# Optimization experiments

Hardware: AMD Instinct MI355X
Metric: run time of the kernel (lower is better)

## Reference

```python
import jax, jax.numpy as jnp
import numpy as np
from jax import lax

DN = ('NCHW', 'OIHW', 'NCHW')

def _dwsep(x, dw, pw_w, pw_b, stride):
    # depthwise: groups = in_channels, kernel (C,1,3,3)
    y = lax.conv_general_dilated(x, dw, (stride, stride), [(1, 1), (1, 1)],
                                 dimension_numbers=DN, feature_group_count=x.shape[1])
    # pointwise 1x1
    y = lax.conv_general_dilated(y, pw_w, (1, 1), 'VALID', dimension_numbers=DN)
    return y + pw_b[None, :, None, None]

def setup_inputs() -> dict:
    key = jax.random.key(0)
    ks = jax.random.split(key, 16)
    s = 0.1
    inp = {
        'flow_raw': jax.random.normal(ks[0], (32, 2, 480, 640), jnp.float32),
        'dw1': jax.random.normal(ks[1], (5, 1, 3, 3), jnp.float32) * s,
        'pw1_w': jax.random.normal(ks[2], (32, 5, 1, 1), jnp.float32) * s,
        'pw1_b': jnp.zeros((32,), jnp.float32),
        'dw2': jax.random.normal(ks[3], (32, 1, 3, 3), jnp.float32) * s,
        'pw2_w': jax.random.normal(ks[4], (64, 32, 1, 1), jnp.float32) * s,
        'pw2_b': jnp.zeros((64,), jnp.float32),
        'dw3': jax.random.normal(ks[5], (64, 1, 3, 3), jnp.float32) * s,
        'pw3_w': jax.random.normal(ks[6], (64, 64, 1, 1), jnp.float32) * s,
        'pw3_b': jnp.zeros((64,), jnp.float32),
        'attn_w': jax.random.normal(ks[7], (1, 64, 1, 1), jnp.float32) * s,
        'attn_b': jnp.zeros((1,), jnp.float32),
        'mlp1_w': jax.random.normal(ks[8], (32, 64), jnp.float32) * s,
        'mlp1_b': jnp.zeros((32,), jnp.float32),
        'mlp2_w': jax.random.normal(ks[9], (3, 32), jnp.float32) * s,
        'mlp2_b': jnp.zeros((3,), jnp.float32),
        'w_ih': jax.random.normal(ks[10], (96, 3), jnp.float32) * s,
        'w_hh': jax.random.normal(ks[11], (96, 32), jnp.float32) * s,
        'b_ih': jnp.zeros((96,), jnp.float32),
        'b_hh': jnp.zeros((96,), jnp.float32),
        'fc_w': jnp.zeros((3, 32), jnp.float32),  # gru_fc init to zero in torch code
        'fc_b': jnp.zeros((3,), jnp.float32),
    }
    return inp

def reference(flow_raw, dw1, pw1_w, pw1_b, dw2, pw2_w, pw2_b, dw3, pw3_w, pw3_b,
              attn_w, attn_b, mlp1_w, mlp1_b, mlp2_w, mlp2_b,
              w_ih, w_hh, b_ih, b_hh, fc_w, fc_b):
    B, _, H, W = flow_raw.shape
    # coordinate channels (x, y, r^2)
    y = jnp.linspace(-1.0, 1.0, H)
    x = jnp.linspace(-1.0, 1.0, W)
    yy, xx = jnp.meshgrid(y, x, indexing='ij')
    coords = jnp.stack([xx, yy, xx**2 + yy**2], axis=0)            # (3,H,W)
    coords_b = jnp.broadcast_to(coords[None], (B, 3, H, W))
    inp = jnp.concatenate([flow_raw, coords_b], axis=1)            # (B,5,H,W)

    f = jax.nn.elu(_dwsep(inp, dw1, pw1_w, pw1_b, 2))              # (B,32,H/2,W/2)
    f = jax.nn.elu(_dwsep(f, dw2, pw2_w, pw2_b, 2))                # (B,64,H/4,W/4)
    f = jax.nn.elu(_dwsep(f, dw3, pw3_w, pw3_b, 2))                # (B,64,H/8,W/8)

    # attention pooling
    logits = jnp.einsum('bchw,oc->bohw', f, attn_w[:, :, 0, 0]) + attn_b[None, :, None, None]
    Bs, _, Hs, Ws = logits.shape
    w = jax.nn.softmax(logits.reshape(Bs, Hs * Ws), axis=-1)       # (B, HW)
    pooled = jnp.einsum('bcn,bn->bc', f.reshape(Bs, 64, Hs * Ws), w)  # (B,64)

    # omega MLP
    h1 = jax.nn.elu(pooled @ mlp1_w.T + mlp1_b)
    omega_inst = h1 @ mlp2_w.T + mlp2_b                            # (B,3)

    # single-step GRU, h0 = 0 (PyTorch gate order: r, z, n)
    h0 = jnp.zeros((B, 32), flow_raw.dtype)
    gi = omega_inst @ w_ih.T + b_ih                                # (B,96)
    gh = h0 @ w_hh.T + b_hh
    i_r, i_z, i_n = jnp.split(gi, 3, axis=-1)
    h_r, h_z, h_n = jnp.split(gh, 3, axis=-1)
    r = jax.nn.sigmoid(i_r + h_r)
    z = jax.nn.sigmoid(i_z + h_z)
    n = jnp.tanh(i_n + r * h_n)
    h = (1.0 - z) * n + z * h0                                     # (B,32)

    delta_omega = h @ fc_w.T + fc_b
    return omega_inst + delta_omega
```

## Files before the change

kernel.cpp:

```cpp
#include <hip/hip_runtime.h>
#include <hip/hip_bf16.h>

#define H0 480
#define W0 640
#define H1 240
#define W1 320
#define H2 120
#define W2 160
#define H3 60
#define W3 80

#define W_PW1T  0
#define W_PW2T  160
#define W_PW3T  2208
#define WBUF_BYTES 65536

#define F2_PB (64 * H2 * W2)
#define F3_PB (64 * H3 * W3)

#define TH 8
#define TW 32
#define TILES_W 5
#define TILES_H 15
#define TILES_PB 75
#define F1COLS 65
#define NP 1105
#define LROW 66
#define LCH 1122

typedef float v2f __attribute__((ext_vector_type(2)));

__global__ __launch_bounds__(256) void k_cvt(
    const float* __restrict__ pw1, const float* __restrict__ pw2,
    const float* __restrict__ pw3, float* __restrict__ wb)
{
    int t = threadIdx.x;
    for (int i = t; i < 160;  i += 256) { int o = i / 5,  c = i % 5;  wb[W_PW1T + c*32 + o] = pw1[i]; }
    for (int i = t; i < 2048; i += 256) { int o = i >> 5, c = i & 31; wb[W_PW2T + c*64 + o] = pw2[i]; }
    for (int i = t; i < 4096; i += 256) { int o = i >> 6, c = i & 63; wb[W_PW3T + c*64 + o] = pw3[i]; }
}

__global__ __launch_bounds__(256, 4) void k_fuse12(
    const float* __restrict__ flow, const float* __restrict__ dw1,
    const float* __restrict__ b1, const float* __restrict__ dw2,
    const float* __restrict__ b2, const float* __restrict__ wb,
    float* __restrict__ out)
{
    __shared__ float f1buf[8 * LCH];

    const int t = threadIdx.x;
    const int bid = blockIdx.x;
    const int b = bid / TILES_PB;
    const int tile = bid - b * TILES_PB;
    const int oh0 = (tile / TILES_W) * TH;
    const int ow0 = (tile % TILES_W) * TW;

    const float sx = 2.f / (W0 - 1), sy = 2.f / (H0 - 1);

    float cs2[3], rs3[3], cs4[3], rs4[3];
    #pragma unroll
    for (int k = 0; k < 3; k++) {
        cs2[k] = dw1[18+k]   + dw1[21+k]   + dw1[24+k];
        rs3[k] = dw1[27+3*k] + dw1[28+3*k] + dw1[29+3*k];
        cs4[k] = dw1[36+k]   + dw1[39+k]   + dw1[42+k];
        rs4[k] = dw1[36+3*k] + dw1[37+3*k] + dw1[38+3*k];
    }
    const float ax2 = 2.f * sx, ay2 = 2.f * sy;
    float ex[3], fyc[3];
    #pragma unroll
    for (int k = 0; k < 3; k++) { ex[k] = sx*(float)(k-1) - 1.f; fyc[k] = sy*(float)(k-1) - 1.f; }
    const float AX1 = ax2*(cs2[0]+cs2[1]+cs2[2]);
    const float AX0 = cs2[0]*ex[0]+cs2[1]*ex[1]+cs2[2]*ex[2];
    const float AY1 = ay2*(rs3[0]+rs3[1]+rs3[2]);
    const float AY0 = rs3[0]*fyc[0]+rs3[1]*fyc[1]+rs3[2]*fyc[2];
    const float GX2 = ax2*ax2*(cs4[0]+cs4[1]+cs4[2]);
    const float GX1 = 2.f*ax2*(cs4[0]*ex[0]+cs4[1]*ex[1]+cs4[2]*ex[2]);
    const float GX0 = cs4[0]*ex[0]*ex[0]+cs4[1]*ex[1]*ex[1]+cs4[2]*ex[2]*ex[2];
    const float GY2 = ay2*ay2*(rs4[0]+rs4[1]+rs4[2]);
    const float GY1 = 2.f*ay2*(rs4[0]*fyc[0]+rs4[1]*fyc[1]+rs4[2]*fyc[2]);
    const float GY0 = rs4[0]*fyc[0]*fyc[0]+rs4[1]*fyc[1]*fyc[1]+rs4[2]*fyc[2]*fyc[2];

    float dd[5][5];
    float vmf[5];
    int   widx[5];
    const float* fb0 = flow + (size_t)(b*2) * (H0*W0);
    const float* fb1 = fb0 + (size_t)(H0*W0);

    #pragma unroll
    for (int i = 0; i < 5; i++) {
        int p = t + i*256; if (p > NP-1) p = NP-1;
        int tr = p / F1COLS;
        int tc = p - tr * F1COLS;
        widx[i] = tr*LROW + (tc & 1)*33 + (tc >> 1);
        int fr = 2*oh0 - 1 + tr;
        int fc = 2*ow0 - 1 + tc;
        vmf[i] = (fr >= 0 && fc >= 0) ? 1.f : 0.f;
        if (fr >= 1 && fc >= 1) {
            const float* r0 = fb0 + (size_t)(2*fr - 1) * W0 + (2*fc - 1);
            const float* r1 = fb1 + (size_t)(2*fr - 1) * W0 + (2*fc - 1);
            float a0 = 0.f, a1 = 0.f;
            #pragma unroll
            for (int ky = 0; ky < 3; ky++)
                #pragma unroll
                for (int kx = 0; kx < 3; kx++) {
                    a0 = fmaf(dw1[ky*3+kx],   r0[ky*W0+kx], a0);
                    a1 = fmaf(dw1[9+ky*3+kx], r1[ky*W0+kx], a1);
                }
            dd[i][0] = a0; dd[i][1] = a1;
            float fcf = (float)fc, frf = (float)fr;
            dd[i][2] = fmaf(AX1, fcf, AX0);
            dd[i][3] = fmaf(AY1, frf, AY0);
            dd[i][4] = fmaf(fmaf(GX2, fcf, GX1), fcf, GX0)
                     + fmaf(fmaf(GY2, frf, GY1), frf, GY0);
        } else {
            int frc = fr < 0 ? 0 : fr, fcc = fc < 0 ? 0 : fc;
            int ih0 = 2*frc - 1, iw0 = 2*fcc - 1;
            float mh[3] = { ih0 >= 0 ? 1.f : 0.f, 1.f, 1.f };
            float mw[3] = { iw0 >= 0 ? 1.f : 0.f, 1.f, 1.f };
            int ihx[3] = { ih0 < 0 ? 0 : ih0, ih0 + 1, ih0 + 2 };
            int iwx[3] = { iw0 < 0 ? 0 : iw0, iw0 + 1, iw0 + 2 };
            float a0 = 0.f, a1 = 0.f;
            #pragma unroll
            for (int ky = 0; ky < 3; ky++) {
                const float* rp0 = fb0 + (size_t)ihx[ky] * W0;
                const float* rp1 = fb1 + (size_t)ihx[ky] * W0;
                #pragma unroll
                for (int kx = 0; kx < 3; kx++) {
                    float m = mh[ky]*mw[kx];
                    a0 = fmaf(dw1[ky*3+kx],   m * rp0[iwx[kx]], a0);
                    a1 = fmaf(dw1[9+ky*3+kx], m * rp1[iwx[kx]], a1);
                }
            }
            dd[i][0] = a0; dd[i][1] = a1;
            float axv = 0.f, ayv = 0.f, arv = 0.f;
            #pragma unroll
            for (int ky = 0; ky < 3; ky++) {
                float yv = fmaf((float)(ih0 + ky), sy, -1.f);
                #pragma unroll
                for (int kx = 0; kx < 3; kx++) {
                    float xv = fmaf((float)(iw0 + kx), sx, -1.f);
                    float m = mh[ky]*mw[kx];
                    axv = fmaf(dw1[18 + ky*3 + kx], m * xv, axv);
                    ayv = fmaf(dw1[27 + ky*3 + kx], m * yv, ayv);
                    arv = fmaf(dw1[36 + ky*3 + kx], m * (xv*xv + yv*yv), arv);
                }
            }
            dd[i][2] = axv; dd[i][3] = ayv; dd[i][4] = arv;
        }
    }

    v2f acc2[32];
    #pragma unroll
    for (int o = 0; o < 32; o++) acc2[o] = *(const v2f*)(b2 + 2*o);

    const int lr = t >> 5, lc = t & 31;
    const int rbase = 2*lr*LROW + lc;

    for (int cc = 0; cc < 4; cc++) {
        #pragma unroll
        for (int j = 0; j < 8; j++) {
            int c = cc*8 + j;
            float w10 = wb[W_PW1T + c];
            float w11 = wb[W_PW1T + 32 + c];
            float w12 = wb[W_PW1T + 64 + c];
            float w13 = wb[W_PW1T + 96 + c];
            float w14 = wb[W_PW1T + 128 + c];
            float bc = b1[c];
            #pragma unroll
            for (int i = 0; i < 5; i++) {
                float v = bc;
                v = fmaf(w10, dd[i][0], v);
                v = fmaf(w11, dd[i][1], v);
                v = fmaf(w12, dd[i][2], v);
                v = fmaf(w13, dd[i][3], v);
                v = fmaf(w14, dd[i][4], v);
                float f = v > 0.f ? v : (__expf(v) - 1.f);
                f *= vmf[i];
                if (i < 4)               f1buf[j*LCH + widx[i]] = f;
                else if (t < NP - 1024)  f1buf[j*LCH + widx[4]] = f;
            }
        }
        __syncthreads();
        #pragma unroll
        for (int j = 0; j < 8; j++) {
            int c = cc*8 + j;
            const float* w9 = dw2 + c*9;
            const float* fp = f1buf + j*LCH + rbase;
            float dv = 0.f;
            #pragma unroll
            for (int r = 0; r < 3; r++) {
                dv = fmaf(w9[r*3+0], fp[r*LROW],      dv);
                dv = fmaf(w9[r*3+1], fp[r*LROW + 33], dv);
                dv = fmaf(w9[r*3+2], fp[r*LROW + 1],  dv);
            }
            const v2f* wr2 = (const v2f*)(wb + W_PW2T + c*64);
            v2f dvv = { dv, dv };
            #pragma unroll
            for (int o = 0; o < 32; o++)
                acc2[o] = __builtin_elementwise_fma(wr2[o], dvv, acc2[o]);
        }
        __syncthreads();
    }

    const int oh = oh0 + lr, ow = ow0 + lc;
    size_t obase = ((size_t)b * 64) * (H2*W2) + (size_t)oh * W2 + ow;
    #pragma unroll
    for (int o = 0; o < 32; o++) {
        float va = acc2[o].x, vb2 = acc2[o].y;
        out[obase + (size_t)(2*o)   * (H2*W2)] = va  > 0.f ? va  : (__expf(va)  - 1.f);
        out[obase + (size_t)(2*o+1) * (H2*W2)] = vb2 > 0.f ? vb2 : (__expf(vb2) - 1.f);
    }
}

__global__ __launch_bounds__(256, 4) void k_stage3(
    const float* __restrict__ in, const float* __restrict__ dw3,
    const float* __restrict__ b3, const float* __restrict__ wb,
    float* __restrict__ out)
{
    int idx = blockIdx.x * 256 + threadIdx.x;
    int ow = idx % W3; int tmp = idx / W3; int oh = tmp % H3; int b = tmp / H3;
    int ih0 = 2*oh - 1, iw0 = 2*ow - 1;
    float mh[3] = { ih0 >= 0 ? 1.f : 0.f, 1.f, 1.f };
    float mw[3] = { iw0 >= 0 ? 1.f : 0.f, 1.f, 1.f };
    int ihx[3] = { ih0 < 0 ? 0 : ih0, ih0 + 1, ih0 + 2 };
    int iwx[3] = { iw0 < 0 ? 0 : iw0, iw0 + 1, iw0 + 2 };
    float m9[9];
    int off[9];
    #pragma unroll
    for (int ky = 0; ky < 3; ky++)
        #pragma unroll
        for (int kx = 0; kx < 3; kx++) {
            m9[ky*3 + kx] = mh[ky] * mw[kx];
            off[ky*3 + kx] = ihx[ky]*W2 + iwx[kx];
        }

    v2f acc2[32];
    #pragma unroll
    for (int o = 0; o < 32; o++) acc2[o] = *(const v2f*)(b3 + 2*o);

    const float* inb = in + (size_t)b * F2_PB;
    for (int c = 0; c < 64; c++) {
        const float* g = inb + (size_t)c * (H2*W2);
        const float* w9 = dw3 + c*9;
        float dv = 0.f;
        #pragma unroll
        for (int p = 0; p < 9; p++)
            dv = fmaf(w9[p], m9[p] * g[off[p]], dv);
        const v2f* wr2 = (const v2f*)(wb + W_PW3T + c*64);
        v2f dvv = { dv, dv };
        #pragma unroll
        for (int o = 0; o < 32; o++)
            acc2[o] = __builtin_elementwise_fma(wr2[o], dvv, acc2[o]);
    }

    size_t obase = ((size_t)b * 64) * (H3*W3) + (size_t)oh*W3 + ow;
    #pragma unroll
    for (int o = 0; o < 32; o++) {
        float va = acc2[o].x, vb2 = acc2[o].y;
        out[obase + (size_t)(2*o)  *(H3*W3)] = va  > 0.f ? va  : (__expf(va)  - 1.f);
        out[obase + (size_t)(2*o+1)*(H3*W3)] = vb2 > 0.f ? vb2 : (__expf(vb2) - 1.f);
    }
}

__global__ __launch_bounds__(1024) void k_head(
    const float* __restrict__ f3,
    const float* __restrict__ attn_w, const float* __restrict__ attn_b,
    const float* __restrict__ mlp1_w, const float* __restrict__ mlp1_b,
    const float* __restrict__ mlp2_w, const float* __restrict__ mlp2_b,
    const float* __restrict__ w_ih, const float* __restrict__ b_ih,
    const float* __restrict__ b_hh,
    const float* __restrict__ fc_w, const float* __restrict__ fc_b,
    float* __restrict__ out)
{
    const int N  = H3 * W3;
    const int N4 = N / 4;
    __shared__ float s_w[H3 * W3];
    __shared__ float s_attn[64];
    __shared__ float s_redm[16];
    __shared__ float s_reds[16];
    __shared__ float s_inv[1];
    __shared__ float s_pooled[64];
    __shared__ float s_h1[32];
    __shared__ float s_om[3];
    __shared__ float s_h[32];

    int t = threadIdx.x, b = blockIdx.x;
    int lane = t & 63, wid = t >> 6;
    if (t < 64) s_attn[t] = attn_w[t];
    __syncthreads();

    const float4* fb4 = (const float4*)(f3 + (size_t)b * F3_PB);
    float ab = attn_b[0];

    float lmax = -1e30f;
    for (int n4 = t; n4 < N4; n4 += 1024) {
        float4 l = make_float4(ab, ab, ab, ab);
        #pragma unroll 8
        for (int c = 0; c < 64; c++) {
            float4 v = fb4[c * N4 + n4];
            float a = s_attn[c];
            l.x = fmaf(a, v.x, l.x); l.y = fmaf(a, v.y, l.y);
            l.z = fmaf(a, v.z, l.z); l.w = fmaf(a, v.w, l.w);
        }
        ((float4*)s_w)[n4] = l;
        lmax = fmaxf(lmax, fmaxf(fmaxf(l.x, l.y), fmaxf(l.z, l.w)));
    }
    #pragma unroll
    for (int off = 32; off; off >>= 1) lmax = fmaxf(lmax, __shfl_down(lmax, off, 64));
    if (lane == 0) s_redm[wid] = lmax;
    __syncthreads();
    {
        float m = s_redm[0];
        #pragma unroll
        for (int i = 1; i < 16; i++) m = fmaxf(m, s_redm[i]);
        lmax = m;
    }

    float lsum = 0.f;
    for (int n = t; n < N; n += 1024) { float e = __expf(s_w[n] - lmax); s_w[n] = e; lsum += e; }
    #pragma unroll
    for (int off = 32; off; off >>= 1) lsum += __shfl_down(lsum, off, 64);
    if (lane == 0) s_reds[wid] = lsum;
    __syncthreads();
    if (t == 0) {
        float s = 0.f;
        #pragma unroll
        for (int i = 0; i < 16; i++) s += s_reds[i];
        s_inv[0] = 1.f / s;
    }
    __syncthreads();
    float invS = s_inv[0];

    const float4* sw4 = (const float4*)s_w;
    for (int c = wid; c < 64; c += 16) {
        float s = 0.f;
        for (int i = lane; i < N4; i += 64) {
            float4 v = fb4[c * N4 + i];
            float4 w = sw4[i];
            s = fmaf(v.x, w.x, s); s = fmaf(v.y, w.y, s);
            s = fmaf(v.z, w.z, s); s = fmaf(v.w, w.w, s);
        }
        #pragma unroll
        for (int off = 32; off; off >>= 1) s += __shfl_down(s, off, 64);
        if (lane == 0) s_pooled[c] = s * invS;
    }
    __syncthreads();

    if (t < 32) {
        float a = mlp1_b[t];
        #pragma unroll 8
        for (int c = 0; c < 64; c++) a = fmaf(mlp1_w[t*64 + c], s_pooled[c], a);
        s_h1[t] = a > 0.f ? a : (__expf(a) - 1.f);
    }
    __syncthreads();
    if (t < 3) {
        float a = mlp2_b[t];
        for (int j = 0; j < 32; j++) a = fmaf(mlp2_w[t*32 + j], s_h1[j], a);
        s_om[t] = a;
    }
    __syncthreads();
    if (t < 32) {
        float gr = b_ih[t], gz = b_ih[32 + t], gn = b_ih[64 + t];
        #pragma unroll
        for (int k = 0; k < 3; k++) {
            float ok = s_om[k];
            gr = fmaf(w_ih[t*3 + k],        ok, gr);
            gz = fmaf(w_ih[(32 + t)*3 + k], ok, gz);
            gn = fmaf(w_ih[(64 + t)*3 + k], ok, gn);
        }
        float hr = b_hh[t], hz = b_hh[32 + t], hn = b_hh[64 + t];
        float r = 1.f / (1.f + __expf(-(gr + hr)));
        float z = 1.f / (1.f + __expf(-(gz + hz)));
        float nn = tanhf(gn + r * hn);
        s_h[t] = (1.f - z) * nn;
    }
    __syncthreads();
    if (t < 3) {
        float dl = fc_b[t];
        for (int j = 0; j < 32; j++) dl = fmaf(fc_w[t*32 + j], s_h[j], dl);
        out[b*3 + t] = s_om[t] + dl;
    }
}

extern "C" void kernel_launch(void* const* d_in, const int* in_sizes, int n_in,
                              void* d_out, int out_size, void* d_ws, size_t ws_size,
                              hipStream_t stream)
{
    const float* flow = (const float*)d_in[0];
    float* wb = (float*)d_ws;

    float* f2 = (float*)((char*)d_ws + WBUF_BYTES);
    float* f3 = f2 + (size_t)32 * F2_PB;

    k_cvt<<<1, 256, 0, stream>>>(
        (const float*)d_in[2], (const float*)d_in[5], (const float*)d_in[8], wb);

    k_fuse12<<<32 * TILES_PB, 256, 0, stream>>>(
        flow, (const float*)d_in[1], (const float*)d_in[3],
        (const float*)d_in[4], (const float*)d_in[6], wb, f2);

    k_stage3<<<(32*H3*W3)/256, 256, 0, stream>>>(
        f2, (const float*)d_in[7], (const float*)d_in[9], wb, f3);

    k_head<<<32, 1024, 0, stream>>>(f3,
        (const float*)d_in[10], (const float*)d_in[11],
        (const float*)d_in[12], (const float*)d_in[13],
        (const float*)d_in[14], (const float*)d_in[15],
        (const float*)d_in[16], (const float*)d_in[18],
        (const float*)d_in[19], (const float*)d_in[20],
        (const float*)d_in[21], (float*)d_out);
}
```

Baseline: 331.7 us.

## Fuse attention logits into stage3 and split head into parallel softmax/pool kernels

Computes the attention logit per pixel inside the stage-3 epilogue, so the head no longer re-reads all 64 channels of f3 to form logits. The old single 32-block head kernel is split into a softmax kernel, a pooling kernel with one block per (batch, channel), and a small MLP/GRU tail kernel, which spreads the pooling reduction across far more blocks. It also lowers the k_fuse12 occupancy hint from 4 to 3 waves. The split adds two kernel launches and a global-memory round trip for the logits.

```diff
diff --git a/kernel.cpp b/kernel.cpp
--- a/kernel.cpp
+++ b/kernel.cpp
@@ -17,6 +17,7 @@
 
 #define F2_PB (64 * H2 * W2)
 #define F3_PB (64 * H3 * W3)
+#define N3    (H3 * W3)
 
 #define TH 8
 #define TW 32
@@ -40,7 +41,7 @@
     for (int i = t; i < 4096; i += 256) { int o = i >> 6, c = i & 63; wb[W_PW3T + c*64 + o] = pw3[i]; }
 }
 
-__global__ __launch_bounds__(256, 4) void k_fuse12(
+__global__ __launch_bounds__(256, 3) void k_fuse12(
     const float* __restrict__ flow, const float* __restrict__ dw1,
     const float* __restrict__ b1, const float* __restrict__ dw2,
     const float* __restrict__ b2, const float* __restrict__ wb,
@@ -215,7 +216,8 @@
 __global__ __launch_bounds__(256, 4) void k_stage3(
     const float* __restrict__ in, const float* __restrict__ dw3,
     const float* __restrict__ b3, const float* __restrict__ wb,
-    float* __restrict__ out)
+    const float* __restrict__ attn_w, const float* __restrict__ attn_b,
+    float* __restrict__ out, float* __restrict__ lg)
 {
     int idx = blockIdx.x * 256 + threadIdx.x;
     int ow = idx % W3; int tmp = idx / W3; int oh = tmp % H3; int b = tmp / H3;
@@ -254,17 +256,76 @@
     }
 
     size_t obase = ((size_t)b * 64) * (H3*W3) + (size_t)oh*W3 + ow;
+    float logit = attn_b[0];
     #pragma unroll
     for (int o = 0; o < 32; o++) {
         float va = acc2[o].x, vb2 = acc2[o].y;
-        out[obase + (size_t)(2*o)  *(H3*W3)] = va  > 0.f ? va  : (__expf(va)  - 1.f);
-        out[obase + (size_t)(2*o+1)*(H3*W3)] = vb2 > 0.f ? vb2 : (__expf(vb2) - 1.f);
-    }
-}
-
-__global__ __launch_bounds__(1024) void k_head(
-    const float* __restrict__ f3,
-    const float* __restrict__ attn_w, const float* __restrict__ attn_b,
+        float ea = va  > 0.f ? va  : (__expf(va)  - 1.f);
+        float eb = vb2 > 0.f ? vb2 : (__expf(vb2) - 1.f);
+        out[obase + (size_t)(2*o)  *(H3*W3)] = ea;
+        out[obase + (size_t)(2*o+1)*(H3*W3)] = eb;
+        logit = fmaf(attn_w[2*o],   ea, logit);
+        logit = fmaf(attn_w[2*o+1], eb, logit);
+    }
+    lg[b*N3 + oh*W3 + ow] = logit;
+}
+
+__global__ __launch_bounds__(256) void k_softmax(
+    float* __restrict__ lg, float* __restrict__ invs)
+{
+    int b = blockIdx.x, t = threadIdx.x;
+    int lane = t & 63, wid = t >> 6;
+    __shared__ float sm[4], ss[4];
+    float* base = lg + b*N3;
+
+    float m = -1e30f;
+    for (int n = t; n < N3; n += 256) m = fmaxf(m, base[n]);
+    #pragma unroll
+    for (int o = 32; o; o >>= 1) m = fmaxf(m, __shfl_down(m, o, 64));
+    if (lane == 0) sm[wid] = m;
+    __syncthreads();
+    m = fmaxf(fmaxf(sm[0], sm[1]), fmaxf(sm[2], sm[3]));
+
+    float s = 0.f;
+    for (int n = t; n < N3; n += 256) {
+        float e = __expf(base[n] - m);
+        base[n] = e;
+        s += e;
+    }
+    #pragma unroll
+    for (int o = 32; o; o >>= 1) s += __shfl_down(s, o, 64);
+    if (lane == 0) ss[wid] = s;
+    __syncthreads();
+    if (t == 0) invs[b] = 1.f / (ss[0] + ss[1] + ss[2] + ss[3]);
+}
+
+__global__ __launch_bounds__(256) void k_pool(
+    const float* __restrict__ f3, const float* __restrict__ lg,
+    const float* __restrict__ invs, float* __restrict__ pooled)
+{
+    int bc = blockIdx.x;
+    int b = bc >> 6, c = bc & 63;
+    int t = threadIdx.x, lane = t & 63, wid = t >> 6;
+    __shared__ float sr[4];
+
+    const float4* f = (const float4*)(f3 + (size_t)b * F3_PB + (size_t)c * N3);
+    const float4* w = (const float4*)(lg + b*N3);
+
+    float s = 0.f;
+    for (int i = t; i < N3/4; i += 256) {
+        float4 a = f[i], e = w[i];
+        s = fmaf(a.x, e.x, s); s = fmaf(a.y, e.y, s);
+        s = fmaf(a.z, e.z, s); s = fmaf(a.w, e.w, s);
+    }
+    #pragma unroll
+    for (int o = 32; o; o >>= 1) s += __shfl_down(s, o, 64);
+    if (lane == 0) sr[wid] = s;
+    __syncthreads();
+    if (t == 0) pooled[bc] = (sr[0] + sr[1] + sr[2] + sr[3]) * invs[b];
+}
+
+__global__ __launch_bounds__(64) void k_tail(
+    const float* __restrict__ pooled,
     const float* __restrict__ mlp1_w, const float* __restrict__ mlp1_b,
     const float* __restrict__ mlp2_w, const float* __restrict__ mlp2_b,
     const float* __restrict__ w_ih, const float* __restrict__ b_ih,
@@ -272,78 +333,13 @@
     const float* __restrict__ fc_w, const float* __restrict__ fc_b,
     float* __restrict__ out)
 {
-    const int N  = H3 * W3;
-    const int N4 = N / 4;
-    __shared__ float s_w[H3 * W3];
-    __shared__ float s_attn[64];
-    __shared__ float s_redm[16];
-    __shared__ float s_reds[16];
-    __shared__ float s_inv[1];
     __shared__ float s_pooled[64];
     __shared__ float s_h1[32];
     __shared__ float s_om[3];
     __shared__ float s_h[32];
-
     int t = threadIdx.x, b = blockIdx.x;
-    int lane = t & 63, wid = t >> 6;
-    if (t < 64) s_attn[t] = attn_w[t];
-    __syncthreads();
-
-    const float4* fb4 = (const float4*)(f3 + (size_t)b * F3_PB);
-    float ab = attn_b[0];
-
-    float lmax = -1e30f;
-    for (int n4 = t; n4 < N4; n4 += 1024) {
-        float4 l = make_float4(ab, ab, ab, ab);
-        #pragma unroll 8
-        for (int c = 0; c < 64; c++) {
-            float4 v = fb4[c * N4 + n4];
-            float a = s_attn[c];
-            l.x = fmaf(a, v.x, l.x); l.y = fmaf(a, v.y, l.y);
-            l.z = fmaf(a, v.z, l.z); l.w = fmaf(a, v.w, l.w);
-        }
-        ((float4*)s_w)[n4] = l;
-        lmax = fmaxf(lmax, fmaxf(fmaxf(l.x, l.y), fmaxf(l.z, l.w)));
-    }
-    #pragma unroll
-    for (int off = 32; off; off >>= 1) lmax = fmaxf(lmax, __shfl_down(lmax, off, 64));
-    if (lane == 0) s_redm[wid] = lmax;
-    __syncthreads();
-    {
-        float m = s_redm[0];
-        #pragma unroll
-        for (int i = 1; i < 16; i++) m = fmaxf(m, s_redm[i]);
-        lmax = m;
-    }
-
-    float lsum = 0.f;
-    for (int n = t; n < N; n += 1024) { float e = __expf(s_w[n] - lmax); s_w[n] = e; lsum += e; }
-    #pragma unroll
-    for (int off = 32; off; off >>= 1) lsum += __shfl_down(lsum, off, 64);
-    if (lane == 0) s_reds[wid] = lsum;
-    __syncthreads();
-    if (t == 0) {
-        float s = 0.f;
-        #pragma unroll
-        for (int i = 0; i < 16; i++) s += s_reds[i];
-        s_inv[0] = 1.f / s;
-    }
-    __syncthreads();
-    float invS = s_inv[0];
-
-    const float4* sw4 = (const float4*)s_w;
-    for (int c = wid; c < 64; c += 16) {
-        float s = 0.f;
-        for (int i = lane; i < N4; i += 64) {
-            float4 v = fb4[c * N4 + i];
-            float4 w = sw4[i];
-            s = fmaf(v.x, w.x, s); s = fmaf(v.y, w.y, s);
-            s = fmaf(v.z, w.z, s); s = fmaf(v.w, w.w, s);
-        }
-        #pragma unroll
-        for (int off = 32; off; off >>= 1) s += __shfl_down(s, off, 64);
-        if (lane == 0) s_pooled[c] = s * invS;
-    }
+
+    s_pooled[t] = pooled[b*64 + t];
     __syncthreads();
 
     if (t < 32) {
@@ -389,8 +385,11 @@
     const float* flow = (const float*)d_in[0];
     float* wb = (float*)d_ws;
 
-    float* f2 = (float*)((char*)d_ws + WBUF_BYTES);
-    float* f3 = f2 + (size_t)32 * F2_PB;
+    float* f2     = (float*)((char*)d_ws + WBUF_BYTES);
+    float* f3     = f2 + (size_t)32 * F2_PB;
+    float* lg     = f3 + (size_t)32 * F3_PB;
+    float* invs   = lg + (size_t)32 * N3;
+    float* pooled = invs + 32;
 
     k_cvt<<<1, 256, 0, stream>>>(
         (const float*)d_in[2], (const float*)d_in[5], (const float*)d_in[8], wb);
@@ -400,10 +399,14 @@
         (const float*)d_in[4], (const float*)d_in[6], wb, f2);
 
     k_stage3<<<(32*H3*W3)/256, 256, 0, stream>>>(
-        f2, (const float*)d_in[7], (const float*)d_in[9], wb, f3);
-
-    k_head<<<32, 1024, 0, stream>>>(f3,
-        (const float*)d_in[10], (const float*)d_in[11],
+        f2, (const float*)d_in[7], (const float*)d_in[9], wb,
+        (const float*)d_in[10], (const float*)d_in[11], f3, lg);
+
+    k_softmax<<<32, 256, 0, stream>>>(lg, invs);
+
+    k_pool<<<32*64, 256, 0, stream>>>(f3, lg, invs, pooled);
+
+    k_tail<<<32, 64, 0, stream>>>(pooled,
         (const float*)d_in[12], (const float*)d_in[13],
         (const float*)d_in[14], (const float*)d_in[15],
         (const float*)d_in[16], (const float*)d_in[18],
```

Result: faster. 310.7 us (-6.3%).
